# Performance work log

Measured on AMD Instinct MI355X. Metric: run time of the kernel, lower is better.

Reference implementation:

```python
import jax, jax.numpy as jnp
import numpy as np

V, N, D, H, C = 3, 4096, 512, 128, 5  # views, nodes, in_dim, hidden, classes
NEG = -9.0e15   # mask value from original code (-9000000000000000.0)
NEG_SLOPE = 0.25


def _leaky(x, slope):
    return jnp.where(x >= 0, x, slope * x)


def setup_inputs() -> dict:
    key = jax.random.key(0)
    ks = jax.random.split(key, 24)
    g = lambda i, shape, s=0.05: (jax.random.normal(ks[i], shape, dtype=jnp.float32) * s)
    return {
        "data": jax.random.normal(ks[0], (V, N, D), dtype=jnp.float32),
        "adj": jax.random.randint(ks[1], (V, N, N), 0, 2, dtype=jnp.int32),
        "gac_w": g(2, (V, D, H)), "gac_b": g(3, (V, H)),
        "a1": g(4, (V, H)), "a2": g(5, (V, H)),
        "mlp_w": g(6, (V, D, H)), "mlp_b": g(7, (V, H)),
        "q_w": g(8, (V, H, H)), "q_b": g(9, (V, H)),
        "k_w": g(10, (V, H, H)), "k_b": g(11, (V, H)),
        "v_w": g(12, (V, H, H)), "v_b": g(13, (V, H)),
        "fc_w": g(14, (V, H, H)), "fc_b": g(15, (V, H)),
        "conf_w": g(16, (V, H, 1)), "conf_b": g(17, (V, 1)),
        "mm_w": g(18, (V * H, C)), "mm_b": g(19, (C,)),
    }


def reference(data, adj, gac_w, gac_b, a1, a2, mlp_w, mlp_b,
              q_w, q_b, k_w, k_b, v_w, v_b, fc_w, fc_b,
              conf_w, conf_b, mm_w, mm_b):
    # --- GraphAttentionConv (per view, vectorized over v) ---
    h = jnp.einsum('vnd,vdh->vnh', data, gac_w)               # spmm(input, W)
    e1 = jnp.einsum('vnh,vh->vn', h, a1)                      # h @ a1
    e2 = jnp.einsum('vnh,vh->vn', h, a2)                      # h @ a2
    e = _leaky(e1[:, :, None] + e2[:, None, :], NEG_SLOPE)    # [V,N,N] broadcast-add
    e = jnp.where(adj > 0, e, NEG)                            # mask by dense adjacency
    att = jax.nn.softmax(e, axis=-1)                          # row softmax
    feat = jnp.einsum('vnm,vmh->vnh', att, h) + gac_b[:, None, :]
    feat = _leaky(feat, NEG_SLOPE)                            # F.leaky_relu(GAC out, 0.25)
    # residual MLP branch
    feat = feat + jnp.einsum('vnd,vdh->vnh', data, mlp_w) + mlp_b[:, None, :]

    # --- StructureGuidedFeatureEnhancement (n_heads=1): per-node HxH attention ---
    Q = jnp.einsum('vnh,vho->vno', feat, q_w) + q_b[:, None, :]
    K = jnp.einsum('vnh,vho->vno', feat, k_w) + k_b[:, None, :]
    Vv = jnp.einsum('vnh,vho->vno', feat, v_w) + v_b[:, None, :]
    scale = jnp.sqrt(jnp.asarray(H, jnp.float32))
    A = Q[:, :, :, None] * K[:, :, None, :] / scale           # [V,N,H,H] outer product
    A = jax.nn.softmax(A, axis=-1)
    agg = jnp.einsum('vnio,vno->vni', A, Vv)                  # attention @ V
    agg = jnp.einsum('vnh,vho->vno', agg, fc_w) + fc_b[:, None, :]
    feat = jax.nn.relu(agg)

    # --- TCP confidence gating ---
    conf = jnp.einsum('vnh,vho->vno', feat, conf_w) + conf_b[:, None, :]  # [V,N,1]
    feat = feat * conf

    # --- concat views along feature dim, final classifier ---
    mm = jnp.transpose(feat, (1, 0, 2)).reshape(N, V * H)     # [N, V*H]
    return mm @ mm_w + mm_b                                   # MMlogit [N, C]
```

## Files before the change

kernel.cpp:

```cpp
#include <hip/hip_runtime.h>
#include <hip/hip_bf16.h>

#define V 3
#define N 4096
#define D 512
#define H 128
#define C 5
#define KS 4
#define M2 64
#define LOG2E 1.4426950408889634f

typedef short short8 __attribute__((ext_vector_type(8)));
typedef float floatx4 __attribute__((ext_vector_type(4)));
typedef int   intx4  __attribute__((ext_vector_type(4)));

__device__ __forceinline__ unsigned short f2bf(float f){
  __hip_bfloat16 h = __float2bfloat16(f);
  return *reinterpret_cast<unsigned short*>(&h);
}
__device__ __forceinline__ unsigned int pk_bf16(float a, float b){
  unsigned int ua = __float_as_uint(a), ub = __float_as_uint(b);
  ua += 0x7FFFu + ((ua >> 16) & 1u);
  ub += 0x7FFFu + ((ub >> 16) & 1u);
  return (ua >> 16) | (ub & 0xFFFF0000u);
}

#define TN1 16
__global__ __launch_bounds__(256) void k1_gemm(
    const float* __restrict__ data,
    const float* __restrict__ gac_w,
    const float* __restrict__ mlp_w,
    const float* __restrict__ a1, const float* __restrict__ a2,
    unsigned short* __restrict__ hT, float* __restrict__ mlp_out,
    float* __restrict__ e1, float* __restrict__ e2)
{
  const int v = blockIdx.y;
  const int n0 = blockIdx.x * TN1;
  const int t = threadIdx.x;
  const int half = t >> 7, tt = t & 127;
  __shared__ float ds[D][20];
  __shared__ float epart[2][2][TN1];
  float* comb = &ds[0][0];
  const float* dp = data + ((size_t)v*N + n0)*D;
  for (int j = t; j < TN1*D; j += 256){
    int r = j >> 9, d = j & (D-1);
    ds[d][r] = dp[(size_t)r*D + d];
  }
  __syncthreads();
  float ag[TN1], am[TN1];
  #pragma unroll
  for (int r=0;r<TN1;r++){ ag[r]=0.f; am[r]=0.f; }
  const int d0 = half*256;
  const float* gw = gac_w + (size_t)v*D*H + tt;
  const float* mw = mlp_w + (size_t)v*D*H + tt;
  for (int d=d0; d<d0+256; d++){
    float wg = gw[(size_t)d*H];
    float wm = mw[(size_t)d*H];
    const float4* p = (const float4*)&ds[d][0];
    float4 x0=p[0], x1=p[1], x2=p[2], x3=p[3];
    float xv[16] = {x0.x,x0.y,x0.z,x0.w, x1.x,x1.y,x1.z,x1.w,
                    x2.x,x2.y,x2.z,x2.w, x3.x,x3.y,x3.z,x3.w};
    #pragma unroll
    for (int r=0;r<TN1;r++){
      ag[r] = fmaf(xv[r], wg, ag[r]);
      am[r] = fmaf(xv[r], wm, am[r]);
    }
  }
  __syncthreads();
  if (half == 1){
    #pragma unroll
    for (int r=0;r<TN1;r++){
      comb[r*H + tt]          = ag[r];
      comb[TN1*H + r*H + tt]  = am[r];
    }
  }
  __syncthreads();
  if (half == 0){
    float* mp = mlp_out + ((size_t)v*N + n0)*H + tt;
    unsigned short pk[TN1];
    const float a1v = a1[v*H + tt], a2v = a2[v*H + tt];
    #pragma unroll
    for (int r=0;r<TN1;r++){
      ag[r] += comb[r*H + tt];
      am[r] += comb[TN1*H + r*H + tt];
      mp[(size_t)r*H] = am[r];
      pk[r] = f2bf(ag[r]);
    }
    uint4* hp = (uint4*)(hT + ((size_t)v*H + tt)*N + n0);
    hp[0] = *(uint4*)&pk[0];
    hp[1] = *(uint4*)&pk[8];
    #pragma unroll
    for (int r=0;r<TN1;r++){
      float s1 = ag[r]*a1v, s2 = ag[r]*a2v;
      #pragma unroll
      for (int o=32;o>0;o>>=1){ s1 += __shfl_down(s1,o); s2 += __shfl_down(s2,o); }
      if ((tt&63)==0){ epart[0][tt>>6][r]=s1; epart[1][tt>>6][r]=s2; }
    }
  }
  __syncthreads();
  if (t < TN1)        e1[(size_t)v*N + n0 + t]       = LOG2E*(epart[0][0][t]    + epart[0][1][t]);
  else if (t < 2*TN1) e2[(size_t)v*N + n0 + (t-TN1)] = LOG2E*(epart[1][0][t-TN1]+ epart[1][1][t-TN1]);
}

__global__ __launch_bounds__(512, 4) void k2_attn(
    const unsigned short* __restrict__ hT, const int* __restrict__ adj,
    const float* __restrict__ e1g, const float* __restrict__ e2g,
    float* __restrict__ pacc, float* __restrict__ pdenG)
{
  const int v = blockIdx.z;
  const int ksid = blockIdx.y;
  const int n0 = blockIdx.x * M2;
  const int kbase = ksid * (N/KS);
  const int t = threadIdx.x;
  const int w = t >> 6, l = t & 63;
  __shared__ __align__(16) unsigned short Afrag[2][4][4][64][8];
  __shared__ float pden_sh[M2][4];

  const int ksl  = w & 3;
  const int quad = l >> 4;
  const int rt0  = w >> 2;
  const int row0 = rt0*16 + (l & 15);
  const int row1 = row0 + 32;
  const int koff = ksl*32 + quad*8;
  const intx4* ap0 = (const intx4*)(adj + ((size_t)v*N + n0 + row0)*N + kbase + koff);
  const intx4* ap1 = (const intx4*)(adj + ((size_t)v*N + n0 + row1)*N + kbase + koff);
  const float4* ep = (const float4*)(e2g + (size_t)v*N + kbase + koff);
  const float e1r0 = e1g[(size_t)v*N + n0 + row0];
  const float e1r1 = e1g[(size_t)v*N + n0 + row1];
  float psum0 = 0.f, psum1 = 0.f;

  const int col = w*16 + (l & 15);
  const unsigned short* bcol = hT + ((size_t)v*H + col)*N + kbase + quad*8;
  floatx4 acc[4];
  #pragma unroll
  for (int rt=0;rt<4;rt++) acc[rt] = (floatx4){0.f,0.f,0.f,0.f};

  intx4  a00 = __builtin_nontemporal_load(ap0);
  intx4  a01 = __builtin_nontemporal_load(ap0 + 1);
  intx4  a10 = __builtin_nontemporal_load(ap1);
  intx4  a11 = __builtin_nontemporal_load(ap1 + 1);
  float4 ev0 = ep[0];
  float4 ev1 = ep[1];

  const int NCH = (N/KS)/128;
  #pragma unroll 1
  for (int c = 0; c < NCH; c++){
    const int buf = c & 1;
    {
      float ev[8] = {ev0.x,ev0.y,ev0.z,ev0.w, ev1.x,ev1.y,ev1.z,ev1.w};
      int   aa[8] = {a00.x,a00.y,a00.z,a00.w, a01.x,a01.y,a01.z,a01.w};
      int   bb[8] = {a10.x,a10.y,a10.z,a10.w, a11.x,a11.y,a11.z,a11.w};
      float wa[8], wb[8];
      #pragma unroll
      for (int j=0;j<8;j++){
        float ya = e1r0 + ev[j];
        ya = fmaxf(ya, 0.25f*ya);
        float ea = exp2f(ya);
        wa[j] = (aa[j] > 0) ? ea : 0.f;
        psum0 += wa[j];
        float yb = e1r1 + ev[j];
        yb = fmaxf(yb, 0.25f*yb);
        float eb = exp2f(yb);
        wb[j] = (bb[j] > 0) ? eb : 0.f;
        psum1 += wb[j];
      }
      union { short8 s; unsigned int u[4]; } pa, pb;
      #pragma unroll
      for (int j=0;j<4;j++){
        pa.u[j] = pk_bf16(wa[2*j], wa[2*j+1]);
        pb.u[j] = pk_bf16(wb[2*j], wb[2*j+1]);
      }
      *(short8*)&Afrag[buf][rt0  ][ksl][l][0] = pa.s;
      *(short8*)&Afrag[buf][rt0+2][ksl][l][0] = pb.s;
    }
    if (c+1 < NCH){
      a00 = __builtin_nontemporal_load(ap0 + (c+1)*32);
      a01 = __builtin_nontemporal_load(ap0 + (c+1)*32 + 1);
      a10 = __builtin_nontemporal_load(ap1 + (c+1)*32);
      a11 = __builtin_nontemporal_load(ap1 + (c+1)*32 + 1);
      ev0 = ep[(c+1)*32];
      ev1 = ep[(c+1)*32 + 1];
    }
    __syncthreads();
    #pragma unroll
    for (int ks=0; ks<4; ks++){
      short8 b8 = *(const short8*)(bcol + c*128 + ks*32);
      #pragma unroll
      for (int rt=0; rt<4; rt++){
        short8 a8 = *(const short8*)&Afrag[buf][rt][ks][l][0];
        acc[rt] = __builtin_amdgcn_mfma_f32_16x16x32_bf16(a8, b8, acc[rt], 0, 0, 0);
      }
    }
    __syncthreads();
  }
  psum0 += __shfl_xor(psum0, 16);
  psum0 += __shfl_xor(psum0, 32);
  psum1 += __shfl_xor(psum1, 16);
  psum1 += __shfl_xor(psum1, 32);
  if (l < 16){
    pden_sh[row0][ksl] = psum0;
    pden_sh[row1][ksl] = psum1;
  }
  __syncthreads();
  const size_t pb = ((size_t)v*KS + ksid)*(N/M2) + blockIdx.x;
  float* pa = pacc + pb*(M2*H);
  #pragma unroll
  for (int rt=0; rt<4; rt++){
    #pragma unroll
    for (int reg=0; reg<4; reg++){
      const int row = rt*16 + quad*4 + reg;
      pa[row*H + col] = acc[rt][reg];
    }
  }
  if (t < M2){
    float den = pden_sh[t][0] + pden_sh[t][1] + pden_sh[t][2] + pden_sh[t][3];
    pdenG[pb*M2 + t] = den;
  }
}

__global__ __launch_bounds__(512) void k2_reduce(
    const float* __restrict__ pacc, const float* __restrict__ pdenG,
    const float* __restrict__ mlp_out,
    const float* __restrict__ gac_b, const float* __restrict__ mlp_b,
    float* __restrict__ feat)
{
  const int v = blockIdx.y;
  const int n0 = blockIdx.x * M2;
  const int t = threadIdx.x;
  const int col = t & 127, rg = t >> 7;
  size_t pb[KS];
  #pragma unroll
  for (int k=0;k<KS;k++) pb[k] = ((size_t)v*KS + k)*(N/M2) + blockIdx.x;
  const float gb = gac_b[v*H + col];
  const float mb = mlp_b[v*H + col];
  #pragma unroll
  for (int i=0;i<16;i++){
    const int row = rg*16 + i;
    float num = 0.f, den = 0.f;
    #pragma unroll
    for (int k=0;k<KS;k++){
      num += pacc[pb[k]*(M2*H) + row*H + col];
      den += pdenG[pb[k]*M2 + row];
    }
    float x = num/den + gb;
    x = (x >= 0.f) ? x : 0.25f*x;
    const size_t idx = ((size_t)v*N + n0 + row)*H + col;
    feat[idx] = x + mlp_out[idx] + mb;
  }
}

#define TN3 8
__global__ __launch_bounds__(128) void k3_sgfe(
    const float* __restrict__ feat,
    const float* __restrict__ qw, const float* __restrict__ qb,
    const float* __restrict__ kw, const float* __restrict__ kb,
    const float* __restrict__ vw, const float* __restrict__ vb,
    const float* __restrict__ fcw, const float* __restrict__ fcb,
    const float* __restrict__ confw, const float* __restrict__ confb,
    float* __restrict__ feat2)
{
  const int v = blockIdx.y;
  const int n0 = blockIdx.x * TN3;
  const int t = threadIdx.x;
  const int W = t >> 6, lane = t & 63;
  __shared__ float fsT[H][12];
  __shared__ float Qs[TN3][H];
  __shared__ float2 KVs[TN3][H];
  __shared__ float As2T[H][12];
  __shared__ float rbuf2[TN3][2];
  const float* fp = feat + ((size_t)v*N + n0)*H + t;
  #pragma unroll
  for (int r=0;r<TN3;r++) fsT[t][r] = fp[(size_t)r*H];
  __syncthreads();
  const float* qwp = qw + (size_t)v*H*H + t;
  const float* kwp = kw + (size_t)v*H*H + t;
  const float* vwp = vw + (size_t)v*H*H + t;
  float Qr[TN3], Kr[TN3], Vr[TN3];
  {
    const float qbv = qb[v*H+t], kbv = kb[v*H+t], vbv = vb[v*H+t];
    #pragma unroll
    for (int r=0;r<TN3;r++){ Qr[r]=qbv; Kr[r]=kbv; Vr[r]=vbv; }
  }
  for (int i=0;i<H;i++){
    float wq = qwp[(size_t)i*H];
    float wk = kwp[(size_t)i*H];
    float wv = vwp[(size_t)i*H];
    float4 f0 = *(const float4*)&fsT[i][0];
    float4 f1 = *(const float4*)&fsT[i][4];
    float fv[8] = {f0.x,f0.y,f0.z,f0.w, f1.x,f1.y,f1.z,f1.w};
    #pragma unroll
    for (int r=0;r<TN3;r++){
      Qr[r] = fmaf(fv[r], wq, Qr[r]);
      Kr[r] = fmaf(fv[r], wk, Kr[r]);
      Vr[r] = fmaf(fv[r], wv, Vr[r]);
    }
  }
  #pragma unroll
  for (int r=0;r<TN3;r++){
    Qs[r][t] = Qr[r];
    KVs[r][t] = make_float2(Kr[r], Vr[r]);
  }
  __syncthreads();
  const float invs = 0.08838834764831845f;
  #pragma unroll
  for (int p=0;p<4;p++){
    const int r = 2*p + W;
    const float qa = Qs[r][lane]   * invs;
    const float qb2 = Qs[r][lane+64] * invs;
    float sA=0.f, aA=0.f, sB=0.f, aB=0.f;
    const float4* kvp = (const float4*)&KVs[r][0];
    #pragma unroll 4
    for (int oo=0; oo<H/2; oo++){
      float4 kv2 = kvp[oo];
      float eA0 = __expf(qa*kv2.x);  sA += eA0; aA = fmaf(eA0, kv2.y, aA);
      float eA1 = __expf(qa*kv2.z);  sA += eA1; aA = fmaf(eA1, kv2.w, aA);
      float eB0 = __expf(qb2*kv2.x); sB += eB0; aB = fmaf(eB0, kv2.y, aB);
      float eB1 = __expf(qb2*kv2.z); sB += eB1; aB = fmaf(eB1, kv2.w, aB);
    }
    As2T[lane][r]    = aA/sA;
    As2T[lane+64][r] = aB/sB;
  }
  __syncthreads();
  const float* fcwp = fcw + (size_t)v*H*H + t;
  const float fcbv = fcb[v*H+t];
  float g[TN3];
  #pragma unroll
  for (int r=0;r<TN3;r++) g[r] = fcbv;
  for (int i=0;i<H;i++){
    float fw = fcwp[(size_t)i*H];
    float4 a0 = *(const float4*)&As2T[i][0];
    float4 a1v = *(const float4*)&As2T[i][4];
    g[0] = fmaf(a0.x, fw, g[0]);  g[1] = fmaf(a0.y, fw, g[1]);
    g[2] = fmaf(a0.z, fw, g[2]);  g[3] = fmaf(a0.w, fw, g[3]);
    g[4] = fmaf(a1v.x, fw, g[4]); g[5] = fmaf(a1v.y, fw, g[5]);
    g[6] = fmaf(a1v.z, fw, g[6]); g[7] = fmaf(a1v.w, fw, g[7]);
  }
  const float cwv = confw[v*H+t];
  const float cbv = confb[v];
  #pragma unroll
  for (int r=0;r<TN3;r++){
    g[r] = fmaxf(g[r], 0.f);
    float psm = g[r]*cwv;
    #pragma unroll
    for (int o=32;o>0;o>>=1) psm += __shfl_down(psm,o);
    if (lane==0) rbuf2[r][W] = psm;
  }
  __syncthreads();
  #pragma unroll
  for (int r=0;r<TN3;r++){
    const float conf = rbuf2[r][0] + rbuf2[r][1] + cbv;
    feat2[((size_t)v*N + n0 + r)*H + t] = g[r]*conf;
  }
}

__global__ __launch_bounds__(64) void k4_cls(
    const float* __restrict__ feat2,
    const float* __restrict__ mm_w, const float* __restrict__ mm_b,
    float* __restrict__ out)
{
  const int n = blockIdx.x, t = threadIdx.x;
  float a[C] = {0,0,0,0,0};
  for (int j=t; j<V*H; j+=64){
    int vv = j >> 7, hh = j & (H-1);
    float f = feat2[((size_t)vv*N + n)*H + hh];
    #pragma unroll
    for (int c=0;c<C;c++) a[c] = fmaf(f, mm_w[j*C+c], a[c]);
  }
  #pragma unroll
  for (int c=0;c<C;c++){
    #pragma unroll
    for (int o=32;o>0;o>>=1) a[c] += __shfl_down(a[c],o);
  }
  if (t==0){
    #pragma unroll
    for (int c=0;c<C;c++) out[(size_t)n*C+c] = a[c] + mm_b[c];
  }
}

extern "C" void kernel_launch(void* const* d_in, const int* in_sizes, int n_in,
                              void* d_out, int out_size, void* d_ws, size_t ws_size,
                              hipStream_t stream)
{
  (void)in_sizes; (void)n_in; (void)out_size; (void)ws_size;
  const float* data  = (const float*)d_in[0];
  const int*   adj   = (const int*)d_in[1];
  const float* gac_w = (const float*)d_in[2];
  const float* gac_b = (const float*)d_in[3];
  const float* a1    = (const float*)d_in[4];
  const float* a2    = (const float*)d_in[5];
  const float* mlp_w = (const float*)d_in[6];
  const float* mlp_b = (const float*)d_in[7];
  const float* q_w   = (const float*)d_in[8];
  const float* q_b   = (const float*)d_in[9];
  const float* k_w   = (const float*)d_in[10];
  const float* k_b   = (const float*)d_in[11];
  const float* v_w   = (const float*)d_in[12];
  const float* v_b   = (const float*)d_in[13];
  const float* fc_w  = (const float*)d_in[14];
  const float* fc_b  = (const float*)d_in[15];
  const float* cw    = (const float*)d_in[16];
  const float* cb    = (const float*)d_in[17];
  const float* mm_w  = (const float*)d_in[18];
  const float* mm_b  = (const float*)d_in[19];

  float* ws = (float*)d_ws;
  const size_t VNH = (size_t)V*N*H;
  float* mlp   = ws;
  float* feat  = ws + VNH;
  float* feat2 = ws + 2*VNH;
  float* e1    = ws + 3*VNH;
  float* e2    = e1 + (size_t)V*N;
  unsigned short* hT = (unsigned short*)(e2 + (size_t)V*N);
  float* pacc  = (float*)(hT + VNH);
  float* pden  = pacc + (size_t)V*KS*(N/M2)*M2*H;

  k1_gemm<<<dim3(N/TN1, V), 256, 0, stream>>>(data, gac_w, mlp_w, a1, a2,
                                              hT, mlp, e1, e2);
  k2_attn<<<dim3(N/M2, KS, V), 512, 0, stream>>>(hT, adj, e1, e2, pacc, pden);
  k2_reduce<<<dim3(N/M2, V), 512, 0, stream>>>(pacc, pden, mlp, gac_b, mlp_b, feat);
  k3_sgfe<<<dim3(N/TN3, V), 128, 0, stream>>>(feat, q_w, q_b, k_w, k_b, v_w, v_b,
                                              fc_w, fc_b, cw, cb, feat2);
  k4_cls<<<dim3(N),          64, 0, stream>>>(feat2, mm_w, mm_b, (float*)d_out);
}
```

Before: 475.3 us.

## Move input projections to bf16 MFMA and fuse split-K reduce into SGFE

The input GEMMs (data x gac_w and data x mlp_w) now run on bf16 MFMA instructions instead of fp32 FMA loops. A new small kernel transposes and converts both weight matrices to bf16 first. The separate split-K reduction kernel is removed: k3_sgfe now sums the partial attention numerators and denominators directly and applies bias, leaky ReLU and the residual, which drops one launch and one feature round trip through memory. The cost is lower precision in the MLP residual branch and in the e1/e2 logits, plus one extra small launch for the weight transpose.

```diff
diff --git a/kernel.cpp b/kernel.cpp
--- a/kernel.cpp
+++ b/kernel.cpp
@@ -8,6 +8,7 @@
 #define C 5
 #define KS 4
 #define M2 64
+#define M1 32
 #define LOG2E 1.4426950408889634f
 
 typedef short short8 __attribute__((ext_vector_type(8)));
@@ -25,81 +26,132 @@
   return (ua >> 16) | (ub & 0xFFFF0000u);
 }
 
-#define TN1 16
-__global__ __launch_bounds__(256) void k1_gemm(
-    const float* __restrict__ data,
-    const float* __restrict__ gac_w,
-    const float* __restrict__ mlp_w,
+__global__ __launch_bounds__(256) void k0_wt(
+    const float* __restrict__ gw, const float* __restrict__ mw,
+    unsigned short* __restrict__ wT)
+{
+  const int v = blockIdx.x, m = blockIdx.y, kc = blockIdx.z;
+  const int t = threadIdx.x;
+  __shared__ unsigned short tr[128*72];
+  const float* src = (m ? mw : gw) + (size_t)v*D*H + (size_t)kc*64*H;
+  for (int i = t; i < 64*128; i += 256){
+    int kk = i >> 7, col = i & 127;
+    tr[col*72 + kk] = f2bf(src[i]);
+  }
+  __syncthreads();
+  const int col = t >> 1, half = t & 1;
+  uint4* dst = (uint4*)(wT + (((size_t)m*V + v)*H + col)*D + kc*64 + half*32);
+  const unsigned short* s = &tr[col*72 + half*32];
+  dst[0] = *(const uint4*)(s);
+  dst[1] = *(const uint4*)(s + 8);
+  dst[2] = *(const uint4*)(s + 16);
+  dst[3] = *(const uint4*)(s + 24);
+}
+
+__global__ __launch_bounds__(512) void k1_gemm(
+    const float* __restrict__ data, const unsigned short* __restrict__ wT,
     const float* __restrict__ a1, const float* __restrict__ a2,
     unsigned short* __restrict__ hT, float* __restrict__ mlp_out,
-    float* __restrict__ e1, float* __restrict__ e2)
+    float* __restrict__ e1g, float* __restrict__ e2g)
 {
   const int v = blockIdx.y;
-  const int n0 = blockIdx.x * TN1;
+  const int n0 = blockIdx.x * M1;
   const int t = threadIdx.x;
-  const int half = t >> 7, tt = t & 127;
-  __shared__ float ds[D][20];
-  __shared__ float epart[2][2][TN1];
-  float* comb = &ds[0][0];
-  const float* dp = data + ((size_t)v*N + n0)*D;
-  for (int j = t; j < TN1*D; j += 256){
-    int r = j >> 9, d = j & (D-1);
-    ds[d][r] = dp[(size_t)r*D + d];
-  }
-  __syncthreads();
-  float ag[TN1], am[TN1];
-  #pragma unroll
-  for (int r=0;r<TN1;r++){ ag[r]=0.f; am[r]=0.f; }
-  const int d0 = half*256;
-  const float* gw = gac_w + (size_t)v*D*H + tt;
-  const float* mw = mlp_w + (size_t)v*D*H + tt;
-  for (int d=d0; d<d0+256; d++){
-    float wg = gw[(size_t)d*H];
-    float wm = mw[(size_t)d*H];
-    const float4* p = (const float4*)&ds[d][0];
-    float4 x0=p[0], x1=p[1], x2=p[2], x3=p[3];
-    float xv[16] = {x0.x,x0.y,x0.z,x0.w, x1.x,x1.y,x1.z,x1.w,
-                    x2.x,x2.y,x2.z,x2.w, x3.x,x3.y,x3.z,x3.w};
-    #pragma unroll
-    for (int r=0;r<TN1;r++){
-      ag[r] = fmaf(xv[r], wg, ag[r]);
-      am[r] = fmaf(xv[r], wm, am[r]);
-    }
-  }
-  __syncthreads();
-  if (half == 1){
-    #pragma unroll
-    for (int r=0;r<TN1;r++){
-      comb[r*H + tt]          = ag[r];
-      comb[TN1*H + r*H + tt]  = am[r];
-    }
-  }
-  __syncthreads();
-  if (half == 0){
-    float* mp = mlp_out + ((size_t)v*N + n0)*H + tt;
-    unsigned short pk[TN1];
-    const float a1v = a1[v*H + tt], a2v = a2[v*H + tt];
-    #pragma unroll
-    for (int r=0;r<TN1;r++){
-      ag[r] += comb[r*H + tt];
-      am[r] += comb[TN1*H + r*H + tt];
-      mp[(size_t)r*H] = am[r];
-      pk[r] = f2bf(ag[r]);
-    }
-    uint4* hp = (uint4*)(hT + ((size_t)v*H + tt)*N + n0);
-    hp[0] = *(uint4*)&pk[0];
-    hp[1] = *(uint4*)&pk[8];
-    #pragma unroll
-    for (int r=0;r<TN1;r++){
-      float s1 = ag[r]*a1v, s2 = ag[r]*a2v;
-      #pragma unroll
-      for (int o=32;o>0;o>>=1){ s1 += __shfl_down(s1,o); s2 += __shfl_down(s2,o); }
-      if ((tt&63)==0){ epart[0][tt>>6][r]=s1; epart[1][tt>>6][r]=s2; }
-    }
-  }
-  __syncthreads();
-  if (t < TN1)        e1[(size_t)v*N + n0 + t]       = LOG2E*(epart[0][0][t]    + epart[0][1][t]);
-  else if (t < 2*TN1) e2[(size_t)v*N + n0 + (t-TN1)] = LOG2E*(epart[1][0][t-TN1]+ epart[1][1][t-TN1]);
+  const int w = t >> 6, l = t & 63;
+  __shared__ __align__(16) unsigned short AT[2][16][64][8];
+  __shared__ float epart[2][M1][4];
+  unsigned short* hTile = &AT[0][0][0][0];
+
+  {
+    const int r = t >> 4, oct = t & 15;
+    const float4* dp = (const float4*)(data + ((size_t)v*N + n0 + r)*D + oct*32);
+    float4 f[8];
+    #pragma unroll
+    for (int i=0;i<8;i++) f[i] = dp[i];
+    #pragma unroll
+    for (int q=0;q<4;q++){
+      uint4 u;
+      u.x = pk_bf16(f[2*q].x,   f[2*q].y);
+      u.y = pk_bf16(f[2*q].z,   f[2*q].w);
+      u.z = pk_bf16(f[2*q+1].x, f[2*q+1].y);
+      u.w = pk_bf16(f[2*q+1].z, f[2*q+1].w);
+      *(uint4*)&AT[r>>4][oct][(r&15) + 16*q][0] = u;
+    }
+  }
+  __syncthreads();
+  const int m = w >> 2, cb = (w & 3)*32;
+  const int quad = l >> 4, c16 = l & 15;
+  const unsigned short* b0 = wT + (((size_t)m*V + v)*H + cb + c16)*D + quad*8;
+  floatx4 acc[2][2];
+  #pragma unroll
+  for (int rt=0;rt<2;rt++) for (int c=0;c<2;c++) acc[rt][c] = (floatx4){0.f,0.f,0.f,0.f};
+  #pragma unroll
+  for (int ks=0; ks<16; ks++){
+    short8 a0 = *(const short8*)&AT[0][ks][l][0];
+    short8 a1f = *(const short8*)&AT[1][ks][l][0];
+    short8 bb0 = *(const short8*)(b0 + ks*32);
+    short8 bb1 = *(const short8*)(b0 + 16*D + ks*32);
+    acc[0][0] = __builtin_amdgcn_mfma_f32_16x16x32_bf16(a0,  bb0, acc[0][0], 0,0,0);
+    acc[1][0] = __builtin_amdgcn_mfma_f32_16x16x32_bf16(a1f, bb0, acc[1][0], 0,0,0);
+    acc[0][1] = __builtin_amdgcn_mfma_f32_16x16x32_bf16(a0,  bb1, acc[0][1], 0,0,0);
+    acc[1][1] = __builtin_amdgcn_mfma_f32_16x16x32_bf16(a1f, bb1, acc[1][1], 0,0,0);
+  }
+  if (m == 1){
+    #pragma unroll
+    for (int rt=0;rt<2;rt++)
+      #pragma unroll
+      for (int c=0;c<2;c++)
+        #pragma unroll
+        for (int reg=0;reg<4;reg++){
+          const int row = rt*16 + quad*4 + reg, col = cb + c*16 + c16;
+          mlp_out[((size_t)v*N + n0 + row)*H + col] = acc[rt][c][reg];
+        }
+  } else {
+    const float a1v0 = a1[v*H + cb + c16],      a2v0 = a2[v*H + cb + c16];
+    const float a1v1 = a1[v*H + cb + 16 + c16], a2v1 = a2[v*H + cb + 16 + c16];
+    #pragma unroll
+    for (int rt=0;rt<2;rt++)
+      #pragma unroll
+      for (int reg=0;reg<4;reg++){
+        float p1 = acc[rt][0][reg]*a1v0 + acc[rt][1][reg]*a1v1;
+        float p2 = acc[rt][0][reg]*a2v0 + acc[rt][1][reg]*a2v1;
+        p1 += __shfl_xor(p1,1); p1 += __shfl_xor(p1,2);
+        p1 += __shfl_xor(p1,4); p1 += __shfl_xor(p1,8);
+        p2 += __shfl_xor(p2,1); p2 += __shfl_xor(p2,2);
+        p2 += __shfl_xor(p2,4); p2 += __shfl_xor(p2,8);
+        if (c16 == 0){
+          epart[0][rt*16 + quad*4 + reg][w] = p1;
+          epart[1][rt*16 + quad*4 + reg][w] = p2;
+        }
+      }
+  }
+  __syncthreads();
+  if (m == 0){
+    #pragma unroll
+    for (int rt=0;rt<2;rt++)
+      #pragma unroll
+      for (int c=0;c<2;c++)
+        #pragma unroll
+        for (int reg=0;reg<4;reg++){
+          const int row = rt*16 + quad*4 + reg, col = cb + c*16 + c16;
+          hTile[col*40 + row] = f2bf(acc[rt][c][reg]);
+        }
+  }
+  __syncthreads();
+  if (t < 128){
+    const unsigned short* s = &hTile[t*40];
+    uint4* dst = (uint4*)(hT + ((size_t)v*H + t)*N + n0);
+    dst[0] = *(const uint4*)(s);
+    dst[1] = *(const uint4*)(s + 8);
+    dst[2] = *(const uint4*)(s + 16);
+    dst[3] = *(const uint4*)(s + 24);
+  } else if (t < 128 + M1){
+    const int r = t - 128;
+    e1g[(size_t)v*N + n0 + r] = LOG2E*(epart[0][r][0]+epart[0][r][1]+epart[0][r][2]+epart[0][r][3]);
+  } else if (t < 128 + 2*M1){
+    const int r = t - 128 - M1;
+    e2g[(size_t)v*N + n0 + r] = LOG2E*(epart[1][r][0]+epart[1][r][1]+epart[1][r][2]+epart[1][r][3]);
+  }
 }
 
 __global__ __launch_bounds__(512, 4) void k2_attn(
@@ -218,40 +270,11 @@
   }
 }
 
-__global__ __launch_bounds__(512) void k2_reduce(
+#define TN3 8
+__global__ __launch_bounds__(128) void k3_sgfe(
     const float* __restrict__ pacc, const float* __restrict__ pdenG,
     const float* __restrict__ mlp_out,
     const float* __restrict__ gac_b, const float* __restrict__ mlp_b,
-    float* __restrict__ feat)
-{
-  const int v = blockIdx.y;
-  const int n0 = blockIdx.x * M2;
-  const int t = threadIdx.x;
-  const int col = t & 127, rg = t >> 7;
-  size_t pb[KS];
-  #pragma unroll
-  for (int k=0;k<KS;k++) pb[k] = ((size_t)v*KS + k)*(N/M2) + blockIdx.x;
-  const float gb = gac_b[v*H + col];
-  const float mb = mlp_b[v*H + col];
-  #pragma unroll
-  for (int i=0;i<16;i++){
-    const int row = rg*16 + i;
-    float num = 0.f, den = 0.f;
-    #pragma unroll
-    for (int k=0;k<KS;k++){
-      num += pacc[pb[k]*(M2*H) + row*H + col];
-      den += pdenG[pb[k]*M2 + row];
-    }
-    float x = num/den + gb;
-    x = (x >= 0.f) ? x : 0.25f*x;
-    const size_t idx = ((size_t)v*N + n0 + row)*H + col;
-    feat[idx] = x + mlp_out[idx] + mb;
-  }
-}
-
-#define TN3 8
-__global__ __launch_bounds__(128) void k3_sgfe(
-    const float* __restrict__ feat,
     const float* __restrict__ qw, const float* __restrict__ qb,
     const float* __restrict__ kw, const float* __restrict__ kb,
     const float* __restrict__ vw, const float* __restrict__ vb,
@@ -268,9 +291,26 @@
   __shared__ float2 KVs[TN3][H];
   __shared__ float As2T[H][12];
   __shared__ float rbuf2[TN3][2];
-  const float* fp = feat + ((size_t)v*N + n0)*H + t;
-  #pragma unroll
-  for (int r=0;r<TN3;r++) fsT[t][r] = fp[(size_t)r*H];
+  {
+    const int bx2 = blockIdx.x >> 3;
+    const int lr0 = (blockIdx.x & 7) * TN3;
+    const float gbv = gac_b[v*H + t];
+    const float mbv = mlp_b[v*H + t];
+    #pragma unroll
+    for (int r=0;r<TN3;r++){
+      float num = 0.f, den = 0.f;
+      #pragma unroll
+      for (int ks=0;ks<KS;ks++){
+        const size_t pb = ((size_t)v*KS + ks)*(N/M2) + bx2;
+        num += pacc[pb*(M2*H) + (size_t)(lr0 + r)*H + t];
+        den += pdenG[pb*M2 + lr0 + r];
+      }
+      float x = num/den + gbv;
+      x = (x >= 0.f) ? x : 0.25f*x;
+      x += mlp_out[((size_t)v*N + n0 + r)*H + t] + mbv;
+      fsT[t][r] = x;
+    }
+  }
   __syncthreads();
   const float* qwp = qw + (size_t)v*H*H + t;
   const float* kwp = kw + (size_t)v*H*H + t;
@@ -406,19 +446,19 @@
   float* ws = (float*)d_ws;
   const size_t VNH = (size_t)V*N*H;
   float* mlp   = ws;
-  float* feat  = ws + VNH;
-  float* feat2 = ws + 2*VNH;
-  float* e1    = ws + 3*VNH;
+  float* feat2 = ws + VNH;
+  float* e1    = ws + 2*VNH;
   float* e2    = e1 + (size_t)V*N;
   unsigned short* hT = (unsigned short*)(e2 + (size_t)V*N);
-  float* pacc  = (float*)(hT + VNH);
+  unsigned short* wT = hT + VNH;
+  float* pacc  = (float*)(wT + (size_t)2*V*H*D);
   float* pden  = pacc + (size_t)V*KS*(N/M2)*M2*H;
 
-  k1_gemm<<<dim3(N/TN1, V), 256, 0, stream>>>(data, gac_w, mlp_w, a1, a2,
-                                              hT, mlp, e1, e2);
-  k2_attn<<<dim3(N/M2, KS, V), 512, 0, stream>>>(hT, adj, e1, e2, pacc, pden);
-  k2_reduce<<<dim3(N/M2, V), 512, 0, stream>>>(pacc, pden, mlp, gac_b, mlp_b, feat);
-  k3_sgfe<<<dim3(N/TN3, V), 128, 0, stream>>>(feat, q_w, q_b, k_w, k_b, v_w, v_b,
-                                              fc_w, fc_b, cw, cb, feat2);
-  k4_cls<<<dim3(N),          64, 0, stream>>>(feat2, mm_w, mm_b, (float*)d_out);
-}
+  k0_wt  <<<dim3(V, 2, D/64), 256, 0, stream>>>(gac_w, mlp_w, wT);
+  k1_gemm<<<dim3(N/M1, V),    512, 0, stream>>>(data, wT, a1, a2, hT, mlp, e1, e2);
+  k2_attn<<<dim3(N/M2, KS, V),512, 0, stream>>>(hT, adj, e1, e2, pacc, pden);
+  k3_sgfe<<<dim3(N/TN3, V),   128, 0, stream>>>(pacc, pden, mlp, gac_b, mlp_b,
+                                                q_w, q_b, k_w, k_b, v_w, v_b,
+                                                fc_w, fc_b, cw, cb, feat2);
+  k4_cls <<<dim3(N),           64, 0, stream>>>(feat2, mm_w, mm_b, (float*)d_out);
+}
```

Result: faster. 447.3 us (-5.9%).
